# Performance work log

Hardware: AMD Instinct MI355X
Metric: run time of the kernel (lower is better)

Reference implementation:

```python
import jax, jax.numpy as jnp
import numpy as np

DRUG_DIM, TARGET_DIM, HEADS, DIM_HEAD = 768, 2560, 8, 96
INNER = HEADS * DIM_HEAD
NEG = -1000000.0
LN_EPS = 1e-5


def setup_inputs() -> dict:
    key = jax.random.key(0)
    ks = jax.random.split(key, 10)
    b, n, m = 16, 256, 1024
    drug = jax.random.normal(ks[0], (b, n, DRUG_DIM), dtype=jnp.float32)
    target = jax.random.normal(ks[1], (b, m, TARGET_DIM), dtype=jnp.float32)
    drug_mask = jax.random.randint(ks[2], (b, n), 0, 2, dtype=jnp.int32)
    pro_mask = jax.random.randint(ks[3], (b, m), 0, 2, dtype=jnp.int32)
    # parameters (torch Linear weight is (out,in); store as (in,out) for x @ W)
    Wq = jax.random.normal(ks[4], (DRUG_DIM, INNER), dtype=jnp.float32) / np.sqrt(DRUG_DIM)
    Wk = jax.random.normal(ks[5], (TARGET_DIM, INNER), dtype=jnp.float32) / np.sqrt(TARGET_DIM)
    Wv = jax.random.normal(ks[6], (TARGET_DIM, INNER), dtype=jnp.float32) / np.sqrt(TARGET_DIM)
    Wo = jax.random.normal(ks[7], (INNER, DRUG_DIM), dtype=jnp.float32) / np.sqrt(INNER)
    bo = jnp.zeros((DRUG_DIM,), dtype=jnp.float32)
    gamma = jnp.ones((DRUG_DIM,), dtype=jnp.float32)
    beta = jnp.zeros((DRUG_DIM,), dtype=jnp.float32)
    return {"drug": drug, "target": target, "drug_mask": drug_mask,
            "pro_mask": pro_mask, "Wq": Wq, "Wk": Wk, "Wv": Wv,
            "Wo": Wo, "bo": bo, "gamma": gamma, "beta": beta}


def reference(drug, target, drug_mask, pro_mask, Wq, Wk, Wv, Wo, bo, gamma, beta):
    b, n, _ = drug.shape
    m = target.shape[1]
    scale = DIM_HEAD ** -0.5
    # projections -> (b, h, len, d)
    q = (drug @ Wq).reshape(b, n, HEADS, DIM_HEAD).transpose(0, 2, 1, 3)
    k = (target @ Wk).reshape(b, m, HEADS, DIM_HEAD).transpose(0, 2, 1, 3)
    v = (target @ Wv).reshape(b, m, HEADS, DIM_HEAD).transpose(0, 2, 1, 3)
    dots = jnp.einsum('bhnd,bhmd->bhnm', q, k) * scale
    # dual mask: positions where drug_mask==0 (rows) OR pro_mask==0 (cols) -> -1e6
    valid = (drug_mask[:, None, :, None] != 0) & (pro_mask[:, None, None, :] != 0)
    masked_dots = jnp.where(valid, dots, NEG)
    attn = jax.nn.softmax(masked_dots, axis=-1)
    out = jnp.einsum('bhnm,bhmd->bhnd', attn, v)
    out = out.transpose(0, 2, 1, 3).reshape(b, n, INNER)
    out = out @ Wo + bo
    # residual + LayerNorm
    x = out + drug
    mu = jnp.mean(x, axis=-1, keepdims=True)
    var = jnp.mean(jnp.square(x - mu), axis=-1, keepdims=True)
    out = (x - mu) * jax.lax.rsqrt(var + LN_EPS) * gamma + beta
    return (out, attn)
```

## Files before the change

### kernel.cpp

```cpp
#include <hip/hip_runtime.h>

typedef short s16x8 __attribute__((ext_vector_type(8)));
typedef float f32x4 __attribute__((ext_vector_type(4)));

__device__ __forceinline__ unsigned short f2bf(float f) {
    unsigned int u = __builtin_bit_cast(unsigned int, f);
    unsigned int r = u + 0x7FFFu + ((u >> 16) & 1u);
    return (unsigned short)(r >> 16);
}

__device__ __forceinline__ void gload16(const unsigned short* g, unsigned short* l) {
    __builtin_amdgcn_global_load_lds(
        (const __attribute__((address_space(1))) unsigned int*)g,
        (__attribute__((address_space(3))) unsigned int*)l, 16, 0, 0);
}

__global__ __launch_bounds__(256) void cvt_bf16(
    const float* __restrict__ in, unsigned short* __restrict__ out, int n) {
    int i = (blockIdx.x * 256 + threadIdx.x) * 8;
    int stride = gridDim.x * 256 * 8;
    for (; i < n; i += stride) {
        float4 a = *reinterpret_cast<const float4*>(in + i);
        float4 b = *reinterpret_cast<const float4*>(in + i + 4);
        uint4 o;
        o.x = (unsigned int)f2bf(a.x) | ((unsigned int)f2bf(a.y) << 16);
        o.y = (unsigned int)f2bf(a.z) | ((unsigned int)f2bf(a.w) << 16);
        o.z = (unsigned int)f2bf(b.x) | ((unsigned int)f2bf(b.y) << 16);
        o.w = (unsigned int)f2bf(b.z) | ((unsigned int)f2bf(b.w) << 16);
        *reinterpret_cast<uint4*>(out + i) = o;
    }
}

__global__ __launch_bounds__(256) void transpose_bf16(
    const float* __restrict__ W, unsigned short* __restrict__ Wt, int K, int N) {
    __shared__ float t[32][33];
    int k0 = blockIdx.x * 32, n0 = blockIdx.y * 32;
    int tid = threadIdx.x;
    int r = tid >> 5, c = tid & 31;
    for (int p = 0; p < 4; ++p)
        t[p * 8 + r][c] = W[(size_t)(k0 + p * 8 + r) * N + n0 + c];
    __syncthreads();
    for (int p = 0; p < 4; ++p)
        Wt[(size_t)(n0 + p * 8 + r) * K + k0 + c] = f2bf(t[c][p * 8 + r]);
}

__global__ __launch_bounds__(256, 2) void gemm_kv128(
    const unsigned short* __restrict__ A, const unsigned short* __restrict__ Bt,
    int M, int N, int K,
    unsigned short* __restrict__ outA, unsigned short* __restrict__ outVt,
    int seqlen) {
    extern __shared__ __align__(16) unsigned short smem[];
    unsigned short* As = smem;
    unsigned short* Bs = smem + 16384;

    int tid = threadIdx.x, wid = tid >> 6, lane = tid & 63;
    int nb = N / 128;
    int nwg = gridDim.x, bid = blockIdx.x;
    int wg = (bid & 7) * (nwg >> 3) + (bid >> 3);
    int tm = wg / nb, tn = wg % nb;
    int m0 = tm * 128, n0 = tn * 128;
    int wm = (wid >> 1) * 64, wn = (wid & 1) * 64;
    int lrow = lane & 15, lkc = lane >> 4;

    int lrsub = lane >> 3;
    int gch = (lane & 7) ^ lrsub;
    const unsigned short* gA[4];
    const unsigned short* gB[4];
    unsigned short* lA[4];
    unsigned short* lB[4];
    for (int p = 0; p < 4; ++p) {
        int r = (wid * 4 + p) * 8 + lrsub;
        gA[p] = A + (size_t)(m0 + r) * K + gch * 8;
        gB[p] = Bt + (size_t)(n0 + r) * K + gch * 8;
        lA[p] = As + (wid * 4 + p) * 512;
        lB[p] = Bs + (wid * 4 + p) * 512;
    }

    int offA[2][4], offB[2][4];
    for (int kh = 0; kh < 2; ++kh)
        for (int i = 0; i < 4; ++i) {
            int ra = wm + i * 16 + lrow;
            offA[kh][i] = ra * 64 + (((kh * 4 + lkc) ^ (ra & 7)) * 8);
            int rb = wn + i * 16 + lrow;
            offB[kh][i] = rb * 64 + (((kh * 4 + lkc) ^ (rb & 7)) * 8);
        }

    int NT = K / 64;
    f32x4 acc[4][4] = {};

    for (int p = 0; p < 4; ++p) { gload16(gA[p], lA[p]); gload16(gB[p], lB[p]); }

    int cur = 0;
    for (int t = 0; t < NT; ++t) {
        __syncthreads();
        if (t + 1 < NT) {
            int nxt = (cur ^ 1) * 8192;
            int koff = (t + 1) * 64;
            for (int p = 0; p < 4; ++p) {
                gload16(gA[p] + koff, lA[p] + nxt);
                gload16(gB[p] + koff, lB[p] + nxt);
            }
        }
        const unsigned short* Ab = As + cur * 8192;
        const unsigned short* Bb = Bs + cur * 8192;
#pragma unroll
        for (int kh = 0; kh < 2; ++kh) {
            s16x8 af[4], bfv[4];
#pragma unroll
            for (int i = 0; i < 4; ++i) af[i] = *reinterpret_cast<const s16x8*>(&Ab[offA[kh][i]]);
#pragma unroll
            for (int j = 0; j < 4; ++j) bfv[j] = *reinterpret_cast<const s16x8*>(&Bb[offB[kh][j]]);
#pragma unroll
            for (int i = 0; i < 4; ++i)
#pragma unroll
                for (int j = 0; j < 4; ++j)
                    acc[i][j] = __builtin_amdgcn_mfma_f32_16x16x32_bf16(af[i], bfv[j], acc[i][j], 0, 0, 0);
        }
        cur ^= 1;
    }

    int orow4 = (lane >> 4) * 4;
    int bblk = m0 / seqlen;
    for (int i = 0; i < 4; ++i)
        for (int j = 0; j < 4; ++j)
            for (int r = 0; r < 4; ++r) {
                int row = m0 + wm + i * 16 + orow4 + r;
                int col = n0 + wn + j * 16 + lrow;
                int s = row - bblk * seqlen;
                unsigned short hv = f2bf(acc[i][j][r]);
                if (col < 768) {
                    int h = col / 96, d = col - h * 96;
                    outA[(((size_t)(bblk * 8 + h)) * seqlen + s) * 96 + d] = hv;
                } else {
                    int cc = col - 768;
                    int h = cc / 96, d = cc - h * 96;
                    outVt[(((size_t)(bblk * 8 + h)) * 96 + d) * seqlen + s] = hv;
                }
            }
}

template <int OUTMODE>
__global__ __launch_bounds__(256) void gemm_a16(
    const unsigned short* __restrict__ A, const unsigned short* __restrict__ Bt,
    int M, int N, int K,
    float* __restrict__ Cf,
    unsigned short* __restrict__ outA, unsigned short* __restrict__ outVt,
    int seqlen) {
    __shared__ __align__(16) unsigned short As[128 * 32];
    __shared__ __align__(16) unsigned short Bs[128 * 32];
    int tid = threadIdx.x, wid = tid >> 6, lane = tid & 63;
    int nb = N / 128;
    int nwg = gridDim.x;
    int bid = blockIdx.x;
    int wg = bid;
    if ((nwg & 7) == 0) wg = (bid & 7) * (nwg >> 3) + (bid >> 3);
    int tm = wg / nb, tn = wg % nb;
    int m0 = tm * 128, n0 = tn * 128;
    int wm = (wid >> 1) * 64, wn = (wid & 1) * 64;
    int lrow = lane & 15, lkc = lane >> 4;

    const unsigned short* gA[2];
    const unsigned short* gB[2];
    unsigned short* lA[2];
    unsigned short* lB[2];
    for (int p = 0; p < 2; ++p) {
        int e = (wid * 2 + p) * 512 + lane * 8;
        int r = e >> 5;
        int ch = (e >> 3) & 3;
        int sc = ch ^ ((r >> 1) & 3);
        gA[p] = A + (size_t)(m0 + r) * K + sc * 8;
        gB[p] = Bt + (size_t)(n0 + r) * K + sc * 8;
        lA[p] = &As[(wid * 2 + p) * 512];
        lB[p] = &Bs[(wid * 2 + p) * 512];
    }
    int offA[4], offB[4];
    for (int i = 0; i < 4; ++i) {
        int ra = wm + i * 16 + lrow;
        offA[i] = ra * 32 + ((lkc ^ ((ra >> 1) & 3)) * 8);
        int rb = wn + i * 16 + lrow;
        offB[i] = rb * 32 + ((lkc ^ ((rb >> 1) & 3)) * 8);
    }

    f32x4 acc[4][4] = {};
    for (int k0 = 0; k0 < K; k0 += 32) {
        __syncthreads();
        gload16(gA[0], lA[0]);
        gload16(gA[1], lA[1]);
        gload16(gB[0], lB[0]);
        gload16(gB[1], lB[1]);
        gA[0] += 32; gA[1] += 32; gB[0] += 32; gB[1] += 32;
        __syncthreads();
        s16x8 af[4], bfv[4];
        for (int i = 0; i < 4; ++i) af[i] = *reinterpret_cast<const s16x8*>(&As[offA[i]]);
        for (int j = 0; j < 4; ++j) bfv[j] = *reinterpret_cast<const s16x8*>(&Bs[offB[j]]);
        for (int i = 0; i < 4; ++i)
            for (int j = 0; j < 4; ++j)
                acc[i][j] = __builtin_amdgcn_mfma_f32_16x16x32_bf16(af[i], bfv[j], acc[i][j], 0, 0, 0);
    }

    int orow4 = (lane >> 4) * 4;
    int bblk = (OUTMODE == 1) ? (m0 / seqlen) : 0;
    for (int i = 0; i < 4; ++i)
        for (int j = 0; j < 4; ++j)
            for (int r = 0; r < 4; ++r) {
                int row = m0 + wm + i * 16 + orow4 + r;
                int col = n0 + wn + j * 16 + lrow;
                float v = acc[i][j][r];
                if constexpr (OUTMODE == 0) {
                    Cf[(size_t)row * N + col] = v;
                } else {
                    int s = row - bblk * seqlen;
                    unsigned short hv = f2bf(v);
                    if (col < 768) {
                        int h = col / 96, d = col - h * 96;
                        outA[(((size_t)(bblk * 8 + h)) * seqlen + s) * 96 + d] = hv;
                    } else {
                        int cc = col - 768;
                        int h = cc / 96, d = cc - h * 96;
                        outVt[(((size_t)(bblk * 8 + h)) * 96 + d) * seqlen + s] = hv;
                    }
                }
            }
}

#define MT 64
__global__ __launch_bounds__(256) void attn_kernel(
    const unsigned short* __restrict__ Qb,
    const unsigned short* __restrict__ Kb,
    const unsigned short* __restrict__ Vt,
    const int* __restrict__ drug_mask,
    const int* __restrict__ pro_mask,
    float* __restrict__ attn_out,
    unsigned short* __restrict__ AO)
{
    constexpr float scale = 0.10206207261596575f;
    __shared__ __align__(16) unsigned short Qs[64][104];
    __shared__ __align__(16) unsigned short Ks[MT][104];
    __shared__ __align__(16) unsigned short Vts[96][MT + 8];
    __shared__ __align__(16) unsigned short Ps[4][16][MT + 8];
    __shared__ float colv[1024];

    int tid = threadIdx.x, wid = tid >> 6, lane = tid & 63;
    int bh = blockIdx.x, nt = blockIdx.y;
    int b = bh >> 3, h = bh & 7;
    const unsigned short* Qg = Qb + (size_t)bh * 256 * 96 + (size_t)nt * 64 * 96;
    const unsigned short* Kg = Kb + (size_t)bh * 1024 * 96;
    const unsigned short* Vg = Vt + (size_t)bh * 96 * 1024;

    for (int idx = tid; idx < 64 * 12; idx += 256) {
        int r = idx / 12, s = idx % 12;
        *reinterpret_cast<uint4*>(&Qs[r][s * 8]) =
            *reinterpret_cast<const uint4*>(&Qg[r * 96 + s * 8]);
    }
    for (int m = tid; m < 1024; m += 256)
        colv[m] = (pro_mask[b * 1024 + m] != 0) ? 1.0f : 0.0f;

    int lrow = lane & 15, lkg = lane >> 4;
    int qrow0 = nt * 64 + wid * 16;
    float rv[4];
    for (int r = 0; r < 4; ++r)
        rv[r] = (drug_mask[b * 256 + qrow0 + lkg * 4 + r] != 0) ? 1.0f : 0.0f;

    __syncthreads();
    s16x8 qa[3];
    for (int kk = 0; kk < 3; ++kk)
        qa[kk] = *reinterpret_cast<const s16x8*>(&Qs[wid * 16 + lrow][kk * 32 + lkg * 8]);

    float mrun[4], srun[4];
    for (int r = 0; r < 4; ++r) { mrun[r] = -3.0e38f; srun[r] = 0.f; }

    for (int mt = 0; mt < 1024; mt += MT) {
        __syncthreads();
        for (int idx = tid; idx < MT * 12; idx += 256) {
            int r = idx / 12, s = idx % 12;
            *reinterpret_cast<uint4*>(&Ks[r][s * 8]) =
                *reinterpret_cast<const uint4*>(&Kg[(size_t)(mt + r) * 96 + s * 8]);
        }
        __syncthreads();
        float sv[MT / 16][4];
        for (int nf = 0; nf < MT / 16; ++nf) {
            f32x4 acc = {};
            for (int kk = 0; kk < 3; ++kk) {
                s16x8 bb = *reinterpret_cast<const s16x8*>(&Ks[nf * 16 + lrow][kk * 32 + lkg * 8]);
                acc = __builtin_amdgcn_mfma_f32_16x16x32_bf16(qa[kk], bb, acc, 0, 0, 0);
            }
            float cv = colv[mt + nf * 16 + lrow];
            for (int r = 0; r < 4; ++r)
                sv[nf][r] = (rv[r] * cv != 0.f) ? acc[r] * scale : -1.0e6f;
        }
        for (int r = 0; r < 4; ++r) {
            float v = sv[0][r];
            for (int nf = 1; nf < MT / 16; ++nf) v = fmaxf(v, sv[nf][r]);
            for (int o = 1; o < 16; o <<= 1) v = fmaxf(v, __shfl_xor(v, o));
            float nm = fmaxf(mrun[r], v);
            float ts = 0.f;
            for (int nf = 0; nf < MT / 16; ++nf) ts += __expf(sv[nf][r] - nm);
            for (int o = 1; o < 16; o <<= 1) ts += __shfl_xor(ts, o);
            srun[r] = srun[r] * __expf(mrun[r] - nm) + ts;
            mrun[r] = nm;
        }
    }
    float sinv[4];
    for (int r = 0; r < 4; ++r) sinv[r] = 1.0f / srun[r];

    f32x4 oacc[6] = {};
    for (int mt = 0; mt < 1024; mt += MT) {
        __syncthreads();
        for (int idx = tid; idx < MT * 12; idx += 256) {
            int r = idx / 12, s = idx % 12;
            *reinterpret_cast<uint4*>(&Ks[r][s * 8]) =
                *reinterpret_cast<const uint4*>(&Kg[(size_t)(mt + r) * 96 + s * 8]);
        }
        for (int idx = tid; idx < 96 * (MT / 8); idx += 256) {
            int r = idx / (MT / 8), s = idx % (MT / 8);
            *reinterpret_cast<uint4*>(&Vts[r][s * 8]) =
                *reinterpret_cast<const uint4*>(&Vg[(size_t)r * 1024 + mt + s * 8]);
        }
        __syncthreads();
        for (int nf = 0; nf < MT / 16; ++nf) {
            f32x4 acc = {};
            for (int kk = 0; kk < 3; ++kk) {
                s16x8 bb = *reinterpret_cast<const s16x8*>(&Ks[nf * 16 + lrow][kk * 32 + lkg * 8]);
                acc = __builtin_amdgcn_mfma_f32_16x16x32_bf16(qa[kk], bb, acc, 0, 0, 0);
            }
            float cv = colv[mt + nf * 16 + lrow];
            for (int r = 0; r < 4; ++r) {
                float sel = (rv[r] * cv != 0.f) ? acc[r] * scale : -1.0e6f;
                float p = __expf(sel - mrun[r]) * sinv[r];
                attn_out[((size_t)bh * 256 + qrow0 + lkg * 4 + r) * 1024 + mt + nf * 16 + lrow] = p;
                Ps[wid][lkg * 4 + r][nf * 16 + lrow] = f2bf(p);
            }
        }
        __syncthreads();
        for (int kk = 0; kk < MT / 32; ++kk) {
            s16x8 pa = *reinterpret_cast<const s16x8*>(&Ps[wid][lrow][kk * 32 + lkg * 8]);
            for (int df = 0; df < 6; ++df) {
                s16x8 vb = *reinterpret_cast<const s16x8*>(&Vts[df * 16 + lrow][kk * 32 + lkg * 8]);
                oacc[df] = __builtin_amdgcn_mfma_f32_16x16x32_bf16(pa, vb, oacc[df], 0, 0, 0);
            }
        }
    }
    for (int df = 0; df < 6; ++df)
        for (int r = 0; r < 4; ++r) {
            int grow = b * 256 + qrow0 + lkg * 4 + r;
            int gcol = h * 96 + df * 16 + lrow;
            AO[(size_t)grow * 768 + gcol] = f2bf(oacc[df][r]);
        }
}

__global__ __launch_bounds__(256) void ln_kernel(
    const float* __restrict__ O, const float* __restrict__ drug,
    const float* __restrict__ bo, const float* __restrict__ gamma,
    const float* __restrict__ beta, float* __restrict__ out) {
    int row = blockIdx.x, tid = threadIdx.x;
    __shared__ float red[4];
    float x[3], s = 0.f;
    for (int i = 0; i < 3; ++i) {
        int j = tid + i * 256;
        x[i] = O[(size_t)row * 768 + j] + bo[j] + drug[(size_t)row * 768 + j];
        s += x[i];
    }
    for (int o = 32; o; o >>= 1) s += __shfl_xor(s, o);
    if ((tid & 63) == 0) red[tid >> 6] = s;
    __syncthreads();
    float mu = (red[0] + red[1] + red[2] + red[3]) * (1.0f / 768.0f);
    float v = 0.f;
    for (int i = 0; i < 3; ++i) { float d = x[i] - mu; v += d * d; }
    for (int o = 32; o; o >>= 1) v += __shfl_xor(v, o);
    __syncthreads();
    if ((tid & 63) == 0) red[tid >> 6] = v;
    __syncthreads();
    float var = (red[0] + red[1] + red[2] + red[3]) * (1.0f / 768.0f);
    float rs = rsqrtf(var + 1e-5f);
    for (int i = 0; i < 3; ++i) {
        int j = tid + i * 256;
        out[(size_t)row * 768 + j] = (x[i] - mu) * rs * gamma[j] + beta[j];
    }
}

extern "C" void kernel_launch(void* const* d_in, const int* in_sizes, int n_in,
                              void* d_out, int out_size, void* d_ws, size_t ws_size,
                              hipStream_t stream) {
    const float* drug   = (const float*)d_in[0];
    const float* target = (const float*)d_in[1];
    const int*   dmask  = (const int*)d_in[2];
    const int*   pmask  = (const int*)d_in[3];
    const float* Wq = (const float*)d_in[4];
    const float* Wk = (const float*)d_in[5];
    const float* Wv = (const float*)d_in[6];
    const float* Wo = (const float*)d_in[7];
    const float* bo = (const float*)d_in[8];
    const float* gm = (const float*)d_in[9];
    const float* bt = (const float*)d_in[10];

    char* w = (char*)d_ws;
    unsigned short* Wtq  = (unsigned short*)(w + 0);
    unsigned short* Wtkv = (unsigned short*)(w + 1179648);
    unsigned short* Wto  = (unsigned short*)(w + 9043968);
    unsigned short* Qb   = (unsigned short*)(w + 10223616);
    unsigned short* Kb   = (unsigned short*)(w + 16515072);
    unsigned short* Vtb  = (unsigned short*)(w + 41680896);
    unsigned short* AO   = (unsigned short*)(w + 66846720);
    float*          Otmp = (float*)(w + 73138176);
    unsigned short* drugb = (unsigned short*)(w + 85721088);

    float* out_ln   = (float*)d_out;
    float* attn_out = (float*)d_out + 3145728;
    unsigned short* targetb = (unsigned short*)attn_out;

    cvt_bf16<<<2048, 256, 0, stream>>>(target, targetb, 41943040);
    cvt_bf16<<<512, 256, 0, stream>>>(drug, drugb, 3145728);

    transpose_bf16<<<dim3(24, 24), 256, 0, stream>>>(Wq, Wtq, 768, 768);
    transpose_bf16<<<dim3(80, 24), 256, 0, stream>>>(Wk, Wtkv, 2560, 768);
    transpose_bf16<<<dim3(80, 24), 256, 0, stream>>>(Wv, Wtkv + (size_t)768 * 2560, 2560, 768);
    transpose_bf16<<<dim3(24, 24), 256, 0, stream>>>(Wo, Wto, 768, 768);

    gemm_kv128<<<1536, 256, 65536, stream>>>(targetb, Wtkv, 16384, 1536, 2560,
                                             Kb, Vtb, 1024);
    gemm_a16<1><<<192, 256, 0, stream>>>(drugb, Wtq, 4096, 768, 768,
                                         nullptr, Qb, nullptr, 256);
    attn_kernel<<<dim3(128, 4), 256, 0, stream>>>(Qb, Kb, Vtb, dmask, pmask, attn_out, AO);
    gemm_a16<0><<<192, 256, 0, stream>>>(AO, Wto, 4096, 768, 768,
                                         Otmp, nullptr, nullptr, 256);
    ln_kernel<<<4096, 256, 0, stream>>>(Otmp, drug, bo, gm, bt, out_ln);
}
```

Before: 359.6 us.

## Split KV GEMM K-tile into half-stages with explicit vmcnt waits and MFMA priority

Restructures the K/V projection GEMM's LDS pipeline. Each 64-wide K tile now lives in two 32-wide sub-buffers with a new XOR swizzle, and the next tile's half is issued before the current half is consumed. Fine-grained s_waitcnt vmcnt counts, a raw s_barrier, sched_barriers and s_setprio around the MFMA block replace the full __syncthreads per tile. The aim is finer-grained overlap of global-to-LDS loads with compute, at the cost of hand-tuned wait counts that must match the issued loads exactly.

```diff
diff --git a/kernel.cpp b/kernel.cpp
--- a/kernel.cpp
+++ b/kernel.cpp
@@ -13,6 +13,10 @@
     __builtin_amdgcn_global_load_lds(
         (const __attribute__((address_space(1))) unsigned int*)g,
         (__attribute__((address_space(3))) unsigned int*)l, 16, 0, 0);
+}
+
+__device__ __forceinline__ s16x8 ldf(const unsigned short* p) {
+    return *reinterpret_cast<const s16x8*>(p);
 }
 
 __global__ __launch_bounds__(256) void cvt_bf16(
@@ -44,14 +48,12 @@
         Wt[(size_t)(n0 + p * 8 + r) * K + k0 + c] = f2bf(t[c][p * 8 + r]);
 }
 
-__global__ __launch_bounds__(256, 2) void gemm_kv128(
+__global__ __launch_bounds__(256, 2) void gemm_kv(
     const unsigned short* __restrict__ A, const unsigned short* __restrict__ Bt,
     int M, int N, int K,
     unsigned short* __restrict__ outA, unsigned short* __restrict__ outVt,
     int seqlen) {
     extern __shared__ __align__(16) unsigned short smem[];
-    unsigned short* As = smem;
-    unsigned short* Bs = smem + 16384;
 
     int tid = threadIdx.x, wid = tid >> 6, lane = tid & 63;
     int nb = N / 128;
@@ -62,62 +64,77 @@
     int wm = (wid >> 1) * 64, wn = (wid & 1) * 64;
     int lrow = lane & 15, lkc = lane >> 4;
 
-    int lrsub = lane >> 3;
-    int gch = (lane & 7) ^ lrsub;
-    const unsigned short* gA[4];
-    const unsigned short* gB[4];
-    unsigned short* lA[4];
-    unsigned short* lB[4];
-    for (int p = 0; p < 4; ++p) {
-        int r = (wid * 4 + p) * 8 + lrsub;
-        gA[p] = A + (size_t)(m0 + r) * K + gch * 8;
-        gB[p] = Bt + (size_t)(n0 + r) * K + gch * 8;
-        lA[p] = As + (wid * 4 + p) * 512;
-        lB[p] = Bs + (wid * 4 + p) * 512;
-    }
-
-    int offA[2][4], offB[2][4];
-    for (int kh = 0; kh < 2; ++kh)
-        for (int i = 0; i < 4; ++i) {
-            int ra = wm + i * 16 + lrow;
-            offA[kh][i] = ra * 64 + (((kh * 4 + lkc) ^ (ra & 7)) * 8);
-            int rb = wn + i * 16 + lrow;
-            offB[kh][i] = rb * 64 + (((kh * 4 + lkc) ^ (rb & 7)) * 8);
-        }
+    int r0 = (wid * 2 + 0) * 16 + (lane >> 2);
+    int r1 = (wid * 2 + 1) * 16 + (lane >> 2);
+    int sc0 = (lane & 3) ^ ((r0 >> 1) & 3);
+    int sc1 = (lane & 3) ^ ((r1 >> 1) & 3);
+    const unsigned short* gA0 = A + (size_t)(m0 + r0) * K + sc0 * 8;
+    const unsigned short* gA1 = A + (size_t)(m0 + r1) * K + sc1 * 8;
+    const unsigned short* gB0 = Bt + (size_t)(n0 + r0) * K + sc0 * 8;
+    const unsigned short* gB1 = Bt + (size_t)(n0 + r1) * K + sc1 * 8;
+    unsigned short* lp0 = smem + (wid * 2 + 0) * 512;
+    unsigned short* lp1 = smem + (wid * 2 + 1) * 512;
+
+#define STAGE(buf, kh, kcol)                                     \
+    {                                                            \
+        int lo_ = ((buf) * 2 + (kh)) * 4096;                     \
+        gload16(gA0 + (kcol), lp0 + lo_);                        \
+        gload16(gA1 + (kcol), lp1 + lo_);                        \
+        gload16(gB0 + (kcol), lp0 + 16384 + lo_);                \
+        gload16(gB1 + (kcol), lp1 + 16384 + lo_);                \
+    }
+
+    int offA[4], offB[4];
+#pragma unroll
+    for (int i = 0; i < 4; ++i) {
+        int ra = wm + i * 16 + lrow;
+        offA[i] = ra * 32 + ((lkc ^ ((ra >> 1) & 3)) * 8);
+        int rb = wn + i * 16 + lrow;
+        offB[i] = rb * 32 + ((lkc ^ ((rb >> 1) & 3)) * 8);
+    }
 
     int NT = K / 64;
     f32x4 acc[4][4] = {};
 
-    for (int p = 0; p < 4; ++p) { gload16(gA[p], lA[p]); gload16(gB[p], lB[p]); }
+    STAGE(0, 0, 0)
+    STAGE(0, 1, 32)
 
     int cur = 0;
     for (int t = 0; t < NT; ++t) {
-        __syncthreads();
-        if (t + 1 < NT) {
-            int nxt = (cur ^ 1) * 8192;
-            int koff = (t + 1) * 64;
-            for (int p = 0; p < 4; ++p) {
-                gload16(gA[p] + koff, lA[p] + nxt);
-                gload16(gB[p] + koff, lB[p] + nxt);
-            }
-        }
-        const unsigned short* Ab = As + cur * 8192;
-        const unsigned short* Bb = Bs + cur * 8192;
+        bool pf = (t + 1 < NT);
+        int kn = (t + 1) * 64;
 #pragma unroll
         for (int kh = 0; kh < 2; ++kh) {
+            if (pf) {
+                if (kh == 0) STAGE(cur ^ 1, 0, kn)
+                else         STAGE(cur ^ 1, 1, kn + 32)
+                asm volatile("s_waitcnt vmcnt(8)" ::: "memory");
+            } else {
+                if (kh == 0) { asm volatile("s_waitcnt vmcnt(4)" ::: "memory"); }
+                else         { asm volatile("s_waitcnt vmcnt(0)" ::: "memory"); }
+            }
+            __builtin_amdgcn_s_barrier();
+            __builtin_amdgcn_sched_barrier(0);
+            const unsigned short* Ab = smem + (cur * 2 + kh) * 4096;
+            const unsigned short* Bb = Ab + 16384;
             s16x8 af[4], bfv[4];
 #pragma unroll
-            for (int i = 0; i < 4; ++i) af[i] = *reinterpret_cast<const s16x8*>(&Ab[offA[kh][i]]);
-#pragma unroll
-            for (int j = 0; j < 4; ++j) bfv[j] = *reinterpret_cast<const s16x8*>(&Bb[offB[kh][j]]);
+            for (int i = 0; i < 4; ++i) af[i] = ldf(&Ab[offA[i]]);
+#pragma unroll
+            for (int j = 0; j < 4; ++j) bfv[j] = ldf(&Bb[offB[j]]);
+            asm volatile("s_waitcnt lgkmcnt(0)" ::: "memory");
+            __builtin_amdgcn_sched_barrier(0);
+            __builtin_amdgcn_s_setprio(1);
 #pragma unroll
             for (int i = 0; i < 4; ++i)
 #pragma unroll
                 for (int j = 0; j < 4; ++j)
                     acc[i][j] = __builtin_amdgcn_mfma_f32_16x16x32_bf16(af[i], bfv[j], acc[i][j], 0, 0, 0);
+            __builtin_amdgcn_s_setprio(0);
         }
         cur ^= 1;
     }
+#undef STAGE
 
     int orow4 = (lane >> 4) * 4;
     int bblk = m0 / seqlen;
@@ -416,8 +433,8 @@
     transpose_bf16<<<dim3(80, 24), 256, 0, stream>>>(Wv, Wtkv + (size_t)768 * 2560, 2560, 768);
     transpose_bf16<<<dim3(24, 24), 256, 0, stream>>>(Wo, Wto, 768, 768);
 
-    gemm_kv128<<<1536, 256, 65536, stream>>>(targetb, Wtkv, 16384, 1536, 2560,
-                                             Kb, Vtb, 1024);
+    gemm_kv<<<1536, 256, 65536, stream>>>(targetb, Wtkv, 16384, 1536, 2560,
+                                          Kb, Vtb, 1024);
     gemm_a16<1><<<192, 256, 0, stream>>>(drugb, Wtq, 4096, 768, 768,
                                          nullptr, Qb, nullptr, 256);
     attn_kernel<<<dim3(128, 4), 256, 0, stream>>>(Qb, Kb, Vtb, dmask, pmask, attn_out, AO);
```

New measurement: 393.4 us. 9.4% more time.
